# Kernel tuning notes

Measured on AMD Instinct MI355X. Metric: run time of the kernel, lower is better.

The kernel has to match this reference:

```python
import jax, jax.numpy as jnp
import numpy as np

D = 1024          # node_vec_size = 16 heads * 64 head_size
HEADS = 16
DH = 64
HID = 4096        # TFM_HIDDEN_SIZE
L = 12            # TFM_NUM_LAYERS
NC = 256          # num concepts present (WMG2_MAX_CONCEPTS)
CSZ = 128         # WMG2_CONCEPT_SIZE
MAX_AGE = 256     # WMG2_MAX_AGE
AGE_V = MAX_AGE + 2  # 258
OBS = 2048
OUT = 512         # WMG2_OUTPUT_LAYER_SIZE
SCALE = 0.02


def setup_inputs() -> dict:
    key = jax.random.key(0)
    ks = iter(jax.random.split(key, 40))
    rn = lambda shape: jax.random.normal(next(ks), shape, dtype=jnp.float32) * SCALE
    inp = {
        'observation': jax.random.normal(next(ks), (OBS,), dtype=jnp.float32),
        'concepts': jax.random.normal(next(ks), (NC, CSZ), dtype=jnp.float32),
        'W_core': rn((D, OBS)), 'b_core': jnp.zeros((D,), jnp.float32),
        'W_cemb': rn((D, CSZ)), 'b_cemb': jnp.zeros((D,), jnp.float32),
        'W_age': rn((D, AGE_V)), 'b_age': jnp.zeros((D,), jnp.float32),
        'Wq': rn((L, D, D)), 'bq': jnp.zeros((L, D), jnp.float32),
        'Wk': rn((L, D, D)), 'bk': jnp.zeros((L, D), jnp.float32),
        'Wv': rn((L, D, D)), 'bv': jnp.zeros((L, D), jnp.float32),
        'Wo': rn((L, D, D)), 'bo': jnp.zeros((L, D), jnp.float32),
        'ln1_g': jnp.ones((L, D), jnp.float32), 'ln1_b': jnp.zeros((L, D), jnp.float32),
        'W1': rn((L, HID, D)), 'b1': jnp.zeros((L, HID), jnp.float32),
        'W2': rn((L, D, HID)), 'b2': jnp.zeros((L, D), jnp.float32),
        'ln2_g': jnp.ones((L, D), jnp.float32), 'ln2_b': jnp.zeros((L, D), jnp.float32),
        'W_concept': rn((CSZ, D)), 'b_concept': jnp.zeros((CSZ,), jnp.float32),
        'W_out': rn((OUT, D)), 'b_out': jnp.zeros((OUT,), jnp.float32),
    }
    return inp


def _layernorm(x, g, b, eps=1e-5):
    m = jnp.mean(x, axis=-1, keepdims=True)
    v = jnp.var(x, axis=-1, keepdims=True)
    return (x - m) * jax.lax.rsqrt(v + eps) * g + b


def _forward(observation, concepts, W_core, b_core, W_cemb, b_cemb, W_age, b_age,
             Wq, bq, Wk, bk, Wv, bv, Wo, bo, ln1_g, ln1_b, W1, b1, W2, b2,
             ln2_g, ln2_b, W_concept, b_concept, W_out, b_out):
    # --- embed observation node ---
    x0 = observation @ W_core.T + b_core                      # [D]
    # --- embed concept nodes, vectorized age embedding ---
    ages = jnp.arange(NC)
    oh = jax.nn.one_hot(jnp.minimum(ages, AGE_V - 1), AGE_V, dtype=jnp.float32)
    oh = oh.at[:, -1].set(ages.astype(jnp.float32) / MAX_AGE)  # age[-1] = age/MAX_AGE
    age_emb = oh @ W_age.T + b_age                             # [NC, D]
    xc = concepts @ W_cemb.T + b_cemb + age_emb                # [NC, D]
    x = jnp.concatenate([x0[None, :], xc], axis=0)             # [S, D], S = 1+NC

    # --- transformer (post-LN encoder), scan over layers ---
    def layer(h, p):
        wq, bq_, wk, bk_, wv, bv_, wo, bo_, g1, be1, w1, b1_, w2, b2_, g2, be2 = p
        S = h.shape[0]
        q = (h @ wq.T + bq_).reshape(S, HEADS, DH)
        k = (h @ wk.T + bk_).reshape(S, HEADS, DH)
        v = (h @ wv.T + bv_).reshape(S, HEADS, DH)
        scores = jnp.einsum('qhd,khd->hqk', q, k) / jnp.sqrt(jnp.float32(DH))
        attn = jax.nn.softmax(scores, axis=-1)
        o = jnp.einsum('hqk,khd->qhd', attn, v).reshape(S, D)
        h = _layernorm(h + (o @ wo.T + bo_), g1, be1)
        f = jax.nn.relu(h @ w1.T + b1_) @ w2.T + b2_
        h = _layernorm(h + f, g2, be2)
        return h, None

    x, _ = jax.lax.scan(layer, x, (Wq, bq, Wk, bk, Wv, bv, Wo, bo,
                                   ln1_g, ln1_b, W1, b1, W2, b2, ln2_g, ln2_b))
    tfm_out = x[0]                                             # [D] (node 0)
    new_concept = jnp.tanh(tfm_out @ W_concept.T + b_concept)  # [CSZ]
    output = jax.nn.relu(tfm_out @ W_out.T + b_out)[None, :]   # [1, OUT]
    return output, new_concept


def reference(observation, concepts, W_core, b_core, W_cemb, b_cemb, W_age, b_age,
              Wq, bq, Wk, bk, Wv, bv, Wo, bo, ln1_g, ln1_b, W1, b1, W2, b2,
              ln2_g, ln2_b, W_concept, b_concept, W_out, b_out):
    return _forward(observation, concepts, W_core, b_core, W_cemb, b_cemb, W_age, b_age,
                    Wq, bq, Wk, bk, Wv, bv, Wo, bo, ln1_g, ln1_b, W1, b1, W2, b2,
                    ln2_g, ln2_b, W_concept, b_concept, W_out, b_out)
```

## Files before the change

### kernel.cpp

```cpp
#include <hip/hip_runtime.h>
#include <hip/hip_bf16.h>
#include <cmath>

constexpr int D     = 1024;
constexpr int HEADS = 16;
constexpr int DH    = 64;
constexpr int HID   = 4096;
constexpr int NL    = 12;
constexpr int NC    = 256;
constexpr int CSZ   = 128;
constexpr int AGE_V = 258;
constexpr int OBS   = 2048;
constexpr int OUTN  = 512;
constexpr int S     = 257;
constexpr int SP    = 288;

typedef __attribute__((ext_vector_type(8))) short bf16x8v;
typedef __attribute__((ext_vector_type(4))) short short4v;
typedef __attribute__((ext_vector_type(4))) float f32x4;

__device__ __forceinline__ short bfc(float x) {
    __hip_bfloat16 h = __float2bfloat16(x);
    return __builtin_bit_cast(short, h);
}
__device__ __forceinline__ void st_bf16x4(short* p, float4 v) {
    short4v s;
    s.x = bfc(v.x); s.y = bfc(v.y); s.z = bfc(v.z); s.w = bfc(v.w);
    *(short4v*)p = s;
}

constexpr int BM = 96, BN = 32, BK = 64, LDT = 72;

template<int EPI>
__device__ __forceinline__ void gemm_core(const short* __restrict__ A,
                                          const float* __restrict__ B,
                                          const float* __restrict__ bias,
                                          void* __restrict__ Cp,
                                          int K, int N, int kbeg, int klen) {
    __shared__ __align__(16) short As[BM * LDT];
    __shared__ __align__(16) short Bs[BN * LDT];
    const int t  = threadIdx.x;
    const int m0 = blockIdx.y * BM;
    const int n0 = blockIdx.x * BN;
    const int ar = t >> 3;
    const int ac = (t & 7) * 8;
    const short* Ab = A + (size_t)(m0 + ar) * K + kbeg + ac;
    const int sr = t >> 4;
    const int sc = (t & 15) * 4;
    const float* Bb = B + (size_t)(n0 + sr) * K + kbeg + sc;

    const int lane = t & 63, wave = t >> 6;
    const int wm = wave >> 1, wn = wave & 1;
    const int fr = lane & 15, quad = lane >> 4;
    const short* Abase = &As[(wm * 48 + fr) * LDT + quad * 8];
    const short* Bbase = &Bs[(wn * 16 + fr) * LDT + quad * 8];

    f32x4 acc[3] = {};

    bf16x8v areg[3];
    float4  breg[2];
    #pragma unroll
    for (int p = 0; p < 3; ++p)
        areg[p] = *(const bf16x8v*)(Ab + (size_t)(p * 32) * K);
    #pragma unroll
    for (int p = 0; p < 2; ++p)
        breg[p] = *(const float4*)(Bb + (size_t)(p * 16) * K);

    for (int k0 = 0; k0 < klen; k0 += BK) {
        __syncthreads();
        #pragma unroll
        for (int p = 0; p < 3; ++p)
            *(bf16x8v*)&As[(p * 32 + ar) * LDT + ac] = areg[p];
        #pragma unroll
        for (int p = 0; p < 2; ++p)
            st_bf16x4(&Bs[(p * 16 + sr) * LDT + sc], breg[p]);
        __syncthreads();
        if (k0 + BK < klen) {
            #pragma unroll
            for (int p = 0; p < 3; ++p)
                areg[p] = *(const bf16x8v*)(Ab + (size_t)(p * 32) * K + (k0 + BK));
            #pragma unroll
            for (int p = 0; p < 2; ++p)
                breg[p] = *(const float4*)(Bb + (size_t)(p * 16) * K + (k0 + BK));
        }
        #pragma unroll
        for (int kt = 0; kt < 2; ++kt) {
            bf16x8v af[3], bf;
            #pragma unroll
            for (int mt = 0; mt < 3; ++mt)
                af[mt] = *(const bf16x8v*)(Abase + mt * 16 * LDT + kt * 32);
            bf = *(const bf16x8v*)(Bbase + kt * 32);
            #pragma unroll
            for (int mt = 0; mt < 3; ++mt)
                acc[mt] = __builtin_amdgcn_mfma_f32_16x16x32_bf16(
                    af[mt], bf, acc[mt], 0, 0, 0);
        }
    }

    #pragma unroll
    for (int mt = 0; mt < 3; ++mt) {
        const int m = m0 + wm * 48 + mt * 16 + quad * 4;
        const int n = n0 + wn * 16 + fr;
        if (EPI == 2) {
            float* C = (float*)Cp;
            #pragma unroll
            for (int r = 0; r < 4; ++r)
                atomicAdd(&C[(size_t)(m + r) * N + n], acc[mt][r]);
        } else if (EPI == 1) {
            short* C = (short*)Cp;
            const float bvv = bias[n];
            #pragma unroll
            for (int r = 0; r < 4; ++r)
                C[(size_t)(m + r) * N + n] = bfc(fmaxf(acc[mt][r] + bvv, 0.f));
        } else {
            float* C = (float*)Cp;
            const float bvv = bias[n];
            #pragma unroll
            for (int r = 0; r < 4; ++r)
                C[(size_t)(m + r) * N + n] = acc[mt][r] + bvv;
        }
    }
}

template<int EPI>
__global__ __launch_bounds__(256, 3)
void gemm_splitk(const short* __restrict__ A, const float* __restrict__ B,
                 const float* __restrict__ bias, void* __restrict__ C,
                 int K, int N, int klen) {
    gemm_core<EPI>(A, B, bias, C, K, N, blockIdx.z * klen, klen);
}

struct QKVArgs {
    const float* B[3];
    const float* bias[3];
    float* C[3];
};

__global__ __launch_bounds__(256, 3)
void gemm_qkv(const short* __restrict__ A, QKVArgs args, int K, int N) {
    const int z = blockIdx.z;
    gemm_core<0>(A, args.B[z], args.bias[z], args.C[z], K, N, 0, K);
}

constexpr int QB = 8, KT = 32, NT = 9;

__global__ __launch_bounds__(512)
void attn_kernel(const float* __restrict__ Q, const float* __restrict__ Km,
                 const float* __restrict__ V, short* __restrict__ O) {
    __shared__ float Ks[KT * 66];
    __shared__ float Vs[KT * 64];
    __shared__ float pw[QB][NT * KT];
    const int h = blockIdx.y;
    const int t = threadIdx.x;
    const int wq = t >> 6, lane = t & 63;
    const int q = blockIdx.x * QB + wq;
    const bool qok = q < S;
    const int k32 = lane & 31, dh2 = lane >> 5;

    float qr[32];
    #pragma unroll
    for (int i = 0; i < 32; ++i)
        qr[i] = qok ? Q[(size_t)q * D + h * DH + dh2 * 32 + i] : 0.f;

    float s[NT];
    for (int tile = 0; tile < NT; ++tile) {
        const int kk0 = tile * KT;
        __syncthreads();
        #pragma unroll
        for (int p = 0; p < 2; ++p) {
            const int idx = t + p * 512;
            const int kr = idx >> 5, c2 = (idx & 31) * 2;
            const int kg = kk0 + kr;
            float2 v = make_float2(0.f, 0.f);
            if (kg < S) v = *(const float2*)&Km[(size_t)kg * D + h * DH + c2];
            *(float2*)&Ks[kr * 66 + c2] = v;
        }
        __syncthreads();
        float dot = 0.f;
        const float* kp = &Ks[k32 * 66 + dh2 * 32];
        #pragma unroll
        for (int i = 0; i < 32; ++i) dot = fmaf(qr[i], kp[i], dot);
        dot += __shfl_xor(dot, 32, 64);
        s[tile] = (kk0 + k32 < S) ? dot * 0.125f : -1e30f;
    }
    float mx = -1e30f;
    #pragma unroll
    for (int j = 0; j < NT; ++j) mx = fmaxf(mx, s[j]);
    #pragma unroll
    for (int off = 32; off; off >>= 1) mx = fmaxf(mx, __shfl_xor(mx, off, 64));
    float sum = 0.f;
    #pragma unroll
    for (int j = 0; j < NT; ++j) {
        const float e = __expf(s[j] - mx);
        s[j] = e;
        sum += e;
    }
    #pragma unroll
    for (int off = 32; off; off >>= 1) sum += __shfl_xor(sum, off, 64);
    sum *= 0.5f;
    const float inv = 1.f / sum;
    if (qok && dh2 == 0) {
        #pragma unroll
        for (int j = 0; j < NT; ++j) pw[wq][j * KT + k32] = s[j] * inv;
    }
    float acc = 0.f;
    for (int tile = 0; tile < NT; ++tile) {
        const int kk0 = tile * KT;
        __syncthreads();
        {
            const int kr = t >> 4, c4 = (t & 15) * 4;
            const int kg = kk0 + kr;
            float4 v = make_float4(0.f, 0.f, 0.f, 0.f);
            if (kg < S) v = *(const float4*)&V[(size_t)kg * D + h * DH + c4];
            *(float4*)&Vs[kr * 64 + c4] = v;
        }
        __syncthreads();
        if (qok) {
            const float* pwp = &pw[wq][kk0];
            #pragma unroll
            for (int k = 0; k < KT; ++k)
                acc = fmaf(pwp[k], Vs[k * 64 + lane], acc);
        }
    }
    if (qok) O[(size_t)q * D + h * DH + lane] = bfc(acc);
}

__global__ __launch_bounds__(256)
void embed_obs_kernel(const float* __restrict__ obs, const float* __restrict__ Wc,
                      const float* __restrict__ bc, const float* __restrict__ bo0,
                      float* __restrict__ H, short* __restrict__ HB,
                      float* __restrict__ T) {
    const int d = blockIdx.x;
    const int t = threadIdx.x;
    const float4* w4 = (const float4*)&Wc[(size_t)d * OBS];
    const float4* o4 = (const float4*)obs;
    float acc = 0.f;
    #pragma unroll
    for (int i = t; i < OBS / 4; i += 256) {
        const float4 a = o4[i];
        const float4 b = w4[i];
        acc = fmaf(a.x, b.x, acc); acc = fmaf(a.y, b.y, acc);
        acc = fmaf(a.z, b.z, acc); acc = fmaf(a.w, b.w, acc);
    }
    __shared__ float red[256];
    red[t] = acc;
    __syncthreads();
    for (int off = 128; off; off >>= 1) {
        if (t < off) red[t] += red[t + off];
        __syncthreads();
    }
    if (t == 0) {
        const float v = red[0] + bc[d];
        H[d] = v;
        HB[d] = bfc(v);
        T[d] = v + bo0[d];
    }
}

__global__ __launch_bounds__(256)
void embed_concepts_kernel(const float* __restrict__ concepts, const float* __restrict__ Wce,
                           const float* __restrict__ bce, const float* __restrict__ Wa,
                           const float* __restrict__ ba, const float* __restrict__ bo0,
                           float* __restrict__ H, short* __restrict__ HB,
                           short* __restrict__ ATT, float* __restrict__ T) {
    const int row = blockIdx.x + 1;
    const int d = blockIdx.y * 256 + threadIdx.x;
    if (row > NC) {
        H[(size_t)row * D + d] = 0.f;
        HB[(size_t)row * D + d] = 0;
        ATT[(size_t)row * D + d] = 0;
        T[(size_t)row * D + d] = bo0[d];
        return;
    }
    const int i = row - 1;
    __shared__ __align__(16) float cs[CSZ];
    if (threadIdx.x < CSZ) cs[threadIdx.x] = concepts[(size_t)i * CSZ + threadIdx.x];
    __syncthreads();
    const float4* w4 = (const float4*)&Wce[(size_t)d * CSZ];
    const float4* c4 = (const float4*)cs;
    float acc = 0.f;
    #pragma unroll
    for (int c = 0; c < CSZ / 4; ++c) {
        const float4 a = c4[c];
        const float4 b = w4[c];
        acc = fmaf(a.x, b.x, acc); acc = fmaf(a.y, b.y, acc);
        acc = fmaf(a.z, b.z, acc); acc = fmaf(a.w, b.w, acc);
    }
    const float age = Wa[(size_t)d * AGE_V + i] +
                      ((float)i / 256.f) * Wa[(size_t)d * AGE_V + (AGE_V - 1)];
    const float v = acc + bce[d] + ba[d] + age;
    H[(size_t)row * D + d] = v;
    HB[(size_t)row * D + d] = bfc(v);
    T[(size_t)row * D + d] = v + bo0[d];
}

__global__ __launch_bounds__(256)
void ln_kernel(const float* __restrict__ X, const float* __restrict__ g,
               const float* __restrict__ b, float* __restrict__ Y,
               short* __restrict__ Yb,
               float* __restrict__ Tinit, const float* __restrict__ nbias) {
    const int r = blockIdx.x;
    const int t = threadIdx.x;
    const float* x = X + (size_t)r * D;
    float sm = 0.f, ss = 0.f;
    float v[4];
    #pragma unroll
    for (int j = 0; j < 4; ++j) {
        const float u = x[t + j * 256];
        v[j] = u;
        sm += u;
        ss = fmaf(u, u, ss);
    }
    __shared__ float r1[256], r2[256];
    r1[t] = sm; r2[t] = ss;
    __syncthreads();
    for (int off = 128; off; off >>= 1) {
        if (t < off) { r1[t] += r1[t + off]; r2[t] += r2[t + off]; }
        __syncthreads();
    }
    const float m   = r1[0] * (1.f / D);
    const float var = r2[0] * (1.f / D) - m * m;
    const float rs  = rsqrtf(var + 1e-5f);
    #pragma unroll
    for (int j = 0; j < 4; ++j) {
        const int idx = t + j * 256;
        const float y = (v[j] - m) * rs * g[idx] + b[idx];
        Y[(size_t)r * D + idx] = y;
        Yb[(size_t)r * D + idx] = bfc(y);
        if (Tinit) Tinit[(size_t)r * D + idx] = y + nbias[idx];
    }
}

__global__ __launch_bounds__(256)
void head_kernel(const float* __restrict__ H, const float* __restrict__ Wout,
                 const float* __restrict__ bout, const float* __restrict__ Wcon,
                 const float* __restrict__ bcon, float* __restrict__ out) {
    const int j = blockIdx.x;
    const int t = threadIdx.x;
    const float* w = (j < OUTN) ? &Wout[(size_t)j * D] : &Wcon[(size_t)(j - OUTN) * D];
    const float4* w4 = (const float4*)w;
    const float4* h4 = (const float4*)H;
    const float4 a = h4[t];
    const float4 b = w4[t];
    float acc = a.x * b.x + a.y * b.y + a.z * b.z + a.w * b.w;
    __shared__ float red[256];
    red[t] = acc;
    __syncthreads();
    for (int off = 128; off; off >>= 1) {
        if (t < off) red[t] += red[t + off];
        __syncthreads();
    }
    if (t == 0) {
        const float v = red[0] + ((j < OUTN) ? bout[j] : bcon[j - OUTN]);
        out[j] = (j < OUTN) ? fmaxf(v, 0.f) : tanhf(v);
    }
}

extern "C" void kernel_launch(void* const* d_in, const int* in_sizes, int n_in,
                              void* d_out, int out_size, void* d_ws, size_t ws_size,
                              hipStream_t stream) {
    (void)in_sizes; (void)n_in; (void)out_size; (void)ws_size;
    const float* obs     = (const float*)d_in[0];
    const float* concepts= (const float*)d_in[1];
    const float* W_core  = (const float*)d_in[2];
    const float* b_core  = (const float*)d_in[3];
    const float* W_cemb  = (const float*)d_in[4];
    const float* b_cemb  = (const float*)d_in[5];
    const float* W_age   = (const float*)d_in[6];
    const float* b_age   = (const float*)d_in[7];
    const float* Wq      = (const float*)d_in[8];
    const float* bq      = (const float*)d_in[9];
    const float* Wk      = (const float*)d_in[10];
    const float* bk      = (const float*)d_in[11];
    const float* Wv      = (const float*)d_in[12];
    const float* bv      = (const float*)d_in[13];
    const float* Wo      = (const float*)d_in[14];
    const float* bo      = (const float*)d_in[15];
    const float* ln1g    = (const float*)d_in[16];
    const float* ln1b    = (const float*)d_in[17];
    const float* W1      = (const float*)d_in[18];
    const float* b1      = (const float*)d_in[19];
    const float* W2      = (const float*)d_in[20];
    const float* b2      = (const float*)d_in[21];
    const float* ln2g    = (const float*)d_in[22];
    const float* ln2b    = (const float*)d_in[23];
    const float* W_con   = (const float*)d_in[24];
    const float* b_con   = (const float*)d_in[25];
    const float* W_out   = (const float*)d_in[26];
    const float* b_out   = (const float*)d_in[27];
    float* outp = (float*)d_out;

    float* ws   = (float*)d_ws;
    float* h    = ws;
    float* tmpA = h    + (size_t)SP * D;
    float* tmpB = tmpA + (size_t)SP * D;
    float* qb   = tmpB + (size_t)SP * D;
    float* kb   = qb   + (size_t)SP * D;
    float* vb   = kb   + (size_t)SP * D;
    short* hb   = (short*)(vb + (size_t)SP * D);
    short* att  = hb  + (size_t)SP * D;
    short* mid  = att + (size_t)SP * D;

    embed_obs_kernel<<<dim3(D), 256, 0, stream>>>(obs, W_core, b_core, bo, h, hb, tmpA);
    embed_concepts_kernel<<<dim3(SP - 1, D / 256), 256, 0, stream>>>(
        concepts, W_cemb, b_cemb, W_age, b_age, bo, h, hb, att, tmpA);

    for (int l = 0; l < NL; ++l) {
        QKVArgs qa;
        qa.B[0] = Wq + (size_t)l * D * D;  qa.bias[0] = bq + (size_t)l * D;  qa.C[0] = qb;
        qa.B[1] = Wk + (size_t)l * D * D;  qa.bias[1] = bk + (size_t)l * D;  qa.C[1] = kb;
        qa.B[2] = Wv + (size_t)l * D * D;  qa.bias[2] = bv + (size_t)l * D;  qa.C[2] = vb;
        gemm_qkv<<<dim3(D / BN, SP / BM, 3), 256, 0, stream>>>(hb, qa, D, D);
        attn_kernel<<<dim3((S + QB - 1) / QB, HEADS), 512, 0, stream>>>(qb, kb, vb, att);
        gemm_splitk<2><<<dim3(D / BN, SP / BM, 4), 256, 0, stream>>>(
            att, Wo + (size_t)l * D * D, nullptr, tmpA, D, D, 256);
        ln_kernel<<<dim3(S), 256, 0, stream>>>(tmpA, ln1g + (size_t)l * D,
                                               ln1b + (size_t)l * D, h, hb,
                                               tmpB, b2 + (size_t)l * D);
        gemm_splitk<1><<<dim3(HID / BN, SP / BM, 1), 256, 0, stream>>>(
            hb, W1 + (size_t)l * HID * D, b1 + (size_t)l * HID, mid, D, HID, D);
        gemm_splitk<2><<<dim3(D / BN, SP / BM, 8), 256, 0, stream>>>(
            mid, W2 + (size_t)l * D * HID, nullptr, tmpB, HID, D, 512);
        float* ti = (l + 1 < NL) ? tmpA : nullptr;
        const float* nb = (l + 1 < NL) ? (bo + (size_t)(l + 1) * D) : nullptr;
        ln_kernel<<<dim3(S), 256, 0, stream>>>(tmpB, ln2g + (size_t)l * D,
                                               ln2b + (size_t)l * D, h, hb, ti, nb);
    }
    head_kernel<<<dim3(OUTN + CSZ), 256, 0, stream>>>(h, W_out, b_out, W_con, b_con, outp);
}
```

Baseline: 1.541 ms.

## Fuse LayerNorm into following GEMM A-loads and merge embed kernels

Removes the standalone layernorm kernels by computing per-row mean and rstd inside the QKV and W1 GEMMs. Those GEMMs then normalize the fp32 residual tile on the fly while converting it to bf16 for the MFMA tiles, and a few blocks also write the residual-plus-next-bias buffer. The two embedding kernels are merged into one launch, the head kernel absorbs the final layernorm, and BK grows from 64 to 128. This cuts launches and intermediate traffic. In exchange, every GEMM block recomputes row statistics redundantly, reads fp32 A instead of bf16, and runs at lower occupancy (launch bounds of 2 instead of 3).

Result: slower. 1.957 ms (+27.0%).

```diff
diff --git a/kernel.cpp b/kernel.cpp
--- a/kernel.cpp
+++ b/kernel.cpp
@@ -29,71 +29,164 @@
     *(short4v*)p = s;
 }
 
-constexpr int BM = 96, BN = 32, BK = 64, LDT = 72;
-
-template<int EPI>
+constexpr int BM = 96, BN = 32, BK = 128, LDT = 136;
+
+template<int EPI, bool LNA>
 __device__ __forceinline__ void gemm_core(const short* __restrict__ A,
-                                          const float* __restrict__ B,
+                                          const float* __restrict__ Xf,
+                                          const float* __restrict__ lng,
+                                          const float* __restrict__ lnb,
+                                          const float* __restrict__ resb,
+                                          float* __restrict__ resd,
+                                          int resid_sub,
+                                          const float* __restrict__ Bm,
                                           const float* __restrict__ bias,
                                           void* __restrict__ Cp,
-                                          int K, int N, int kbeg, int klen) {
+                                          int K, int N, int kbeg, int klen,
+                                          int m0, int n0, int t) {
     __shared__ __align__(16) short As[BM * LDT];
     __shared__ __align__(16) short Bs[BN * LDT];
-    const int t  = threadIdx.x;
-    const int m0 = blockIdx.y * BM;
-    const int n0 = blockIdx.x * BN;
-    const int ar = t >> 3;
-    const int ac = (t & 7) * 8;
-    const short* Ab = A + (size_t)(m0 + ar) * K + kbeg + ac;
-    const int sr = t >> 4;
-    const int sc = (t & 15) * 4;
-    const float* Bb = B + (size_t)(n0 + sr) * K + kbeg + sc;
-
+    __shared__ float s_mu[BM], s_ri[BM];
     const int lane = t & 63, wave = t >> 6;
+    const int ar  = t >> 4;
+    const int ac8 = (t & 15) * 8;
+    const short* Ab = LNA ? nullptr : (A + (size_t)(m0 + ar) * K + kbeg + ac8);
+    const float* Xa = LNA ? (Xf + (size_t)(m0 + ar) * K + kbeg + ac8) : nullptr;
+    const int sr = t >> 5;
+    const int sc = (t & 31) * 4;
+    const float* Bb = Bm + (size_t)(n0 + sr) * K + kbeg + sc;
+
     const int wm = wave >> 1, wn = wave & 1;
     const int fr = lane & 15, quad = lane >> 4;
     const short* Abase = &As[(wm * 48 + fr) * LDT + quad * 8];
     const short* Bbase = &Bs[(wn * 16 + fr) * LDT + quad * 8];
 
     f32x4 acc[3] = {};
-
-    bf16x8v areg[3];
-    float4  breg[2];
-    #pragma unroll
-    for (int p = 0; p < 3; ++p)
-        areg[p] = *(const bf16x8v*)(Ab + (size_t)(p * 32) * K);
-    #pragma unroll
-    for (int p = 0; p < 2; ++p)
-        breg[p] = *(const float4*)(Bb + (size_t)(p * 16) * K);
+    bf16x8v araw[6];
+    float4  aln[12];
+    float4  breg[4];
+
+    if constexpr (LNA) {
+        #pragma unroll
+        for (int p = 0; p < 6; ++p) {
+            const float* src = Xa + (size_t)(p * 16) * K;
+            aln[2 * p]     = *(const float4*)(src);
+            aln[2 * p + 1] = *(const float4*)(src + 4);
+        }
+    } else {
+        #pragma unroll
+        for (int p = 0; p < 6; ++p)
+            araw[p] = *(const bf16x8v*)(Ab + (size_t)(p * 16) * K);
+    }
+    #pragma unroll
+    for (int p = 0; p < 4; ++p)
+        breg[p] = *(const float4*)(Bb + (size_t)(p * 8) * K);
+
+    if constexpr (LNA) {
+        #pragma unroll 2
+        for (int i = 0; i < 24; ++i) {
+            const int r = wave * 24 + i;
+            const float4* xr = (const float4*)(Xf + (size_t)(m0 + r) * K);
+            float sm = 0.f, ss = 0.f;
+            #pragma unroll
+            for (int j = 0; j < 4; ++j) {
+                const float4 x = xr[lane * 4 + j];
+                sm += x.x + x.y + x.z + x.w;
+                ss = fmaf(x.x, x.x, fmaf(x.y, x.y, fmaf(x.z, x.z, fmaf(x.w, x.w, ss))));
+            }
+            #pragma unroll
+            for (int off = 32; off; off >>= 1) {
+                sm += __shfl_xor(sm, off, 64);
+                ss += __shfl_xor(ss, off, 64);
+            }
+            if (lane == 0) {
+                const float mu = sm * (1.f / 1024.f);
+                s_mu[r] = mu;
+                s_ri[r] = rsqrtf(ss * (1.f / 1024.f) - mu * mu + 1e-5f);
+            }
+        }
+        __syncthreads();
+        if (resid_sub >= 0) {
+            const int rbase = resid_sub * 24;
+            #pragma unroll 4
+            for (int i = 0; i < 24; ++i) {
+                const int rl = rbase + i;
+                const int c = t * 4;
+                const float4 x  = *(const float4*)(Xf + (size_t)(m0 + rl) * K + c);
+                const float4 g4 = *(const float4*)(lng + c);
+                const float4 b4 = *(const float4*)(lnb + c);
+                const float4 n4 = *(const float4*)(resb + c);
+                const float mu = s_mu[rl], ri = s_ri[rl];
+                float4 y;
+                y.x = fmaf((x.x - mu) * ri, g4.x, b4.x) + n4.x;
+                y.y = fmaf((x.y - mu) * ri, g4.y, b4.y) + n4.y;
+                y.z = fmaf((x.z - mu) * ri, g4.z, b4.z) + n4.z;
+                y.w = fmaf((x.w - mu) * ri, g4.w, b4.w) + n4.w;
+                *(float4*)(resd + (size_t)(m0 + rl) * D + c) = y;
+            }
+        }
+    }
 
     for (int k0 = 0; k0 < klen; k0 += BK) {
         __syncthreads();
-        #pragma unroll
-        for (int p = 0; p < 3; ++p)
-            *(bf16x8v*)&As[(p * 32 + ar) * LDT + ac] = areg[p];
-        #pragma unroll
-        for (int p = 0; p < 2; ++p)
-            st_bf16x4(&Bs[(p * 16 + sr) * LDT + sc], breg[p]);
+        if constexpr (LNA) {
+            const float4 g0 = *(const float4*)(lng + kbeg + k0 + ac8);
+            const float4 g1 = *(const float4*)(lng + kbeg + k0 + ac8 + 4);
+            const float4 b0 = *(const float4*)(lnb + kbeg + k0 + ac8);
+            const float4 b1 = *(const float4*)(lnb + kbeg + k0 + ac8 + 4);
+            #pragma unroll
+            for (int p = 0; p < 6; ++p) {
+                const int r = p * 16 + ar;
+                const float mu = s_mu[r], ri = s_ri[r];
+                const float4 xa = aln[2 * p], xb = aln[2 * p + 1];
+                bf16x8v o;
+                o[0] = bfc(fmaf((xa.x - mu) * ri, g0.x, b0.x));
+                o[1] = bfc(fmaf((xa.y - mu) * ri, g0.y, b0.y));
+                o[2] = bfc(fmaf((xa.z - mu) * ri, g0.z, b0.z));
+                o[3] = bfc(fmaf((xa.w - mu) * ri, g0.w, b0.w));
+                o[4] = bfc(fmaf((xb.x - mu) * ri, g1.x, b1.x));
+                o[5] = bfc(fmaf((xb.y - mu) * ri, g1.y, b1.y));
+                o[6] = bfc(fmaf((xb.z - mu) * ri, g1.z, b1.z));
+                o[7] = bfc(fmaf((xb.w - mu) * ri, g1.w, b1.w));
+                *(bf16x8v*)&As[r * LDT + ac8] = o;
+            }
+        } else {
+            #pragma unroll
+            for (int p = 0; p < 6; ++p)
+                *(bf16x8v*)&As[(p * 16 + ar) * LDT + ac8] = araw[p];
+        }
+        #pragma unroll
+        for (int p = 0; p < 4; ++p)
+            st_bf16x4(&Bs[(p * 8 + sr) * LDT + sc], breg[p]);
         __syncthreads();
         if (k0 + BK < klen) {
-            #pragma unroll
-            for (int p = 0; p < 3; ++p)
-                areg[p] = *(const bf16x8v*)(Ab + (size_t)(p * 32) * K + (k0 + BK));
-            #pragma unroll
-            for (int p = 0; p < 2; ++p)
-                breg[p] = *(const float4*)(Bb + (size_t)(p * 16) * K + (k0 + BK));
-        }
-        #pragma unroll
-        for (int kt = 0; kt < 2; ++kt) {
-            bf16x8v af[3], bf;
+            if constexpr (LNA) {
+                #pragma unroll
+                for (int p = 0; p < 6; ++p) {
+                    const float* src = Xa + (size_t)(p * 16) * K + (k0 + BK);
+                    aln[2 * p]     = *(const float4*)(src);
+                    aln[2 * p + 1] = *(const float4*)(src + 4);
+                }
+            } else {
+                #pragma unroll
+                for (int p = 0; p < 6; ++p)
+                    araw[p] = *(const bf16x8v*)(Ab + (size_t)(p * 16) * K + (k0 + BK));
+            }
+            #pragma unroll
+            for (int p = 0; p < 4; ++p)
+                breg[p] = *(const float4*)(Bb + (size_t)(p * 8) * K + (k0 + BK));
+        }
+        #pragma unroll
+        for (int kt = 0; kt < 4; ++kt) {
+            bf16x8v af[3], bfv;
             #pragma unroll
             for (int mt = 0; mt < 3; ++mt)
                 af[mt] = *(const bf16x8v*)(Abase + mt * 16 * LDT + kt * 32);
-            bf = *(const bf16x8v*)(Bbase + kt * 32);
+            bfv = *(const bf16x8v*)(Bbase + kt * 32);
             #pragma unroll
             for (int mt = 0; mt < 3; ++mt)
                 acc[mt] = __builtin_amdgcn_mfma_f32_16x16x32_bf16(
-                    af[mt], bf, acc[mt], 0, 0, 0);
+                    af[mt], bfv, acc[mt], 0, 0, 0);
         }
     }
 
@@ -122,31 +215,57 @@
     }
 }
 
-template<int EPI>
-__global__ __launch_bounds__(256, 3)
-void gemm_splitk(const short* __restrict__ A, const float* __restrict__ B,
-                 const float* __restrict__ bias, void* __restrict__ C,
-                 int K, int N, int klen) {
-    gemm_core<EPI>(A, B, bias, C, K, N, blockIdx.z * klen, klen);
-}
-
 struct QKVArgs {
     const float* B[3];
     const float* bias[3];
     float* C[3];
 };
 
+template<int EPI>
 __global__ __launch_bounds__(256, 3)
-void gemm_qkv(const short* __restrict__ A, QKVArgs args, int K, int N) {
+void k_gemm(const short* __restrict__ A, const float* __restrict__ Bm,
+            const float* __restrict__ bias, void* __restrict__ C,
+            int K, int N, int klen) {
+    gemm_core<EPI, false>(A, nullptr, nullptr, nullptr, nullptr, nullptr, -1,
+                          Bm, bias, C, K, N, blockIdx.z * klen, klen,
+                          blockIdx.y * BM, blockIdx.x * BN, threadIdx.x);
+}
+
+__global__ __launch_bounds__(256, 3)
+void k_gemm_qkv(const short* __restrict__ A, QKVArgs args) {
     const int z = blockIdx.z;
-    gemm_core<0>(A, args.B[z], args.bias[z], args.C[z], K, N, 0, K);
+    gemm_core<0, false>(A, nullptr, nullptr, nullptr, nullptr, nullptr, -1,
+                        args.B[z], args.bias[z], args.C[z], D, D, 0, D,
+                        blockIdx.y * BM, blockIdx.x * BN, threadIdx.x);
+}
+
+__global__ __launch_bounds__(256, 2)
+void k_gemm_qkv_ln(const float* __restrict__ X, const float* __restrict__ lng,
+                   const float* __restrict__ lnb, const float* __restrict__ resb,
+                   float* __restrict__ resd, QKVArgs args) {
+    const int z = blockIdx.z;
+    const int rsub = (z == 0 && blockIdx.x < 4) ? (int)blockIdx.x : -1;
+    gemm_core<0, true>(nullptr, X, lng, lnb, resb, resd, rsub,
+                       args.B[z], args.bias[z], args.C[z], D, D, 0, D,
+                       blockIdx.y * BM, blockIdx.x * BN, threadIdx.x);
+}
+
+__global__ __launch_bounds__(256, 2)
+void k_gemm_w1_ln(const float* __restrict__ X, const float* __restrict__ lng,
+                  const float* __restrict__ lnb, const float* __restrict__ resb,
+                  float* __restrict__ resd, const float* __restrict__ Bm,
+                  const float* __restrict__ bias, short* __restrict__ C) {
+    const int rsub = (blockIdx.x < 4) ? (int)blockIdx.x : -1;
+    gemm_core<1, true>(nullptr, X, lng, lnb, resb, resd, rsub,
+                       Bm, bias, C, D, HID, 0, D,
+                       blockIdx.y * BM, blockIdx.x * BN, threadIdx.x);
 }
 
 constexpr int QB = 8, KT = 32, NT = 9;
 
 __global__ __launch_bounds__(512)
-void attn_kernel(const float* __restrict__ Q, const float* __restrict__ Km,
-                 const float* __restrict__ V, short* __restrict__ O) {
+void k_attn(const float* __restrict__ Q, const float* __restrict__ Km,
+            const float* __restrict__ V, short* __restrict__ O) {
     __shared__ float Ks[KT * 66];
     __shared__ float Vs[KT * 64];
     __shared__ float pw[QB][NT * KT];
@@ -226,58 +345,54 @@
 }
 
 __global__ __launch_bounds__(256)
-void embed_obs_kernel(const float* __restrict__ obs, const float* __restrict__ Wc,
-                      const float* __restrict__ bc, const float* __restrict__ bo0,
-                      float* __restrict__ H, short* __restrict__ HB,
-                      float* __restrict__ T) {
-    const int d = blockIdx.x;
+void k_embed(const float* __restrict__ obs, const float* __restrict__ Wc,
+             const float* __restrict__ bc,
+             const float* __restrict__ concepts, const float* __restrict__ Wce,
+             const float* __restrict__ bce, const float* __restrict__ Wa,
+             const float* __restrict__ ba, const float* __restrict__ bo0,
+             short* __restrict__ HB, short* __restrict__ ATT,
+             float* __restrict__ T) {
     const int t = threadIdx.x;
-    const float4* w4 = (const float4*)&Wc[(size_t)d * OBS];
-    const float4* o4 = (const float4*)obs;
-    float acc = 0.f;
-    #pragma unroll
-    for (int i = t; i < OBS / 4; i += 256) {
-        const float4 a = o4[i];
-        const float4 b = w4[i];
-        acc = fmaf(a.x, b.x, acc); acc = fmaf(a.y, b.y, acc);
-        acc = fmaf(a.z, b.z, acc); acc = fmaf(a.w, b.w, acc);
-    }
     __shared__ float red[256];
-    red[t] = acc;
-    __syncthreads();
-    for (int off = 128; off; off >>= 1) {
-        if (t < off) red[t] += red[t + off];
-        __syncthreads();
-    }
-    if (t == 0) {
-        const float v = red[0] + bc[d];
-        H[d] = v;
-        HB[d] = bfc(v);
-        T[d] = v + bo0[d];
-    }
-}
-
-__global__ __launch_bounds__(256)
-void embed_concepts_kernel(const float* __restrict__ concepts, const float* __restrict__ Wce,
-                           const float* __restrict__ bce, const float* __restrict__ Wa,
-                           const float* __restrict__ ba, const float* __restrict__ bo0,
-                           float* __restrict__ H, short* __restrict__ HB,
-                           short* __restrict__ ATT, float* __restrict__ T) {
-    const int row = blockIdx.x + 1;
-    const int d = blockIdx.y * 256 + threadIdx.x;
+    if (blockIdx.x < D) {
+        const int d = blockIdx.x;
+        const float4* w4 = (const float4*)&Wc[(size_t)d * OBS];
+        const float4* o4 = (const float4*)obs;
+        float acc = 0.f;
+        #pragma unroll
+        for (int i = t; i < OBS / 4; i += 256) {
+            const float4 a = o4[i];
+            const float4 b = w4[i];
+            acc = fmaf(a.x, b.x, acc); acc = fmaf(a.y, b.y, acc);
+            acc = fmaf(a.z, b.z, acc); acc = fmaf(a.w, b.w, acc);
+        }
+        red[t] = acc;
+        __syncthreads();
+        for (int off = 128; off; off >>= 1) {
+            if (t < off) red[t] += red[t + off];
+            __syncthreads();
+        }
+        if (t == 0) {
+            const float v = red[0] + bc[d];
+            HB[d] = bfc(v);
+            T[d] = v + bo0[d];
+        }
+        return;
+    }
+    const int j = blockIdx.x - D;
+    const int row = (j % 287) + 1;
+    const int d = (j / 287) * 256 + t;
     if (row > NC) {
-        H[(size_t)row * D + d] = 0.f;
         HB[(size_t)row * D + d] = 0;
         ATT[(size_t)row * D + d] = 0;
         T[(size_t)row * D + d] = bo0[d];
         return;
     }
     const int i = row - 1;
-    __shared__ __align__(16) float cs[CSZ];
-    if (threadIdx.x < CSZ) cs[threadIdx.x] = concepts[(size_t)i * CSZ + threadIdx.x];
+    if (t < CSZ) red[t] = concepts[(size_t)i * CSZ + t];
     __syncthreads();
     const float4* w4 = (const float4*)&Wce[(size_t)d * CSZ];
-    const float4* c4 = (const float4*)cs;
+    const float4* c4 = (const float4*)red;
     float acc = 0.f;
     #pragma unroll
     for (int c = 0; c < CSZ / 4; ++c) {
@@ -289,69 +404,49 @@
     const float age = Wa[(size_t)d * AGE_V + i] +
                       ((float)i / 256.f) * Wa[(size_t)d * AGE_V + (AGE_V - 1)];
     const float v = acc + bce[d] + ba[d] + age;
-    H[(size_t)row * D + d] = v;
     HB[(size_t)row * D + d] = bfc(v);
     T[(size_t)row * D + d] = v + bo0[d];
 }
 
 __global__ __launch_bounds__(256)
-void ln_kernel(const float* __restrict__ X, const float* __restrict__ g,
-               const float* __restrict__ b, float* __restrict__ Y,
-               short* __restrict__ Yb,
-               float* __restrict__ Tinit, const float* __restrict__ nbias) {
-    const int r = blockIdx.x;
+void k_head_ln(const float* __restrict__ X, const float* __restrict__ g,
+               const float* __restrict__ b, const float* __restrict__ Wout,
+               const float* __restrict__ bout, const float* __restrict__ Wcon,
+               const float* __restrict__ bcon, float* __restrict__ out) {
+    const int j = blockIdx.x;
     const int t = threadIdx.x;
-    const float* x = X + (size_t)r * D;
-    float sm = 0.f, ss = 0.f;
-    float v[4];
-    #pragma unroll
-    for (int j = 0; j < 4; ++j) {
-        const float u = x[t + j * 256];
-        v[j] = u;
-        sm += u;
-        ss = fmaf(u, u, ss);
-    }
     __shared__ float r1[256], r2[256];
+    const float4 x = ((const float4*)X)[t];
+    float sm = x.x + x.y + x.z + x.w;
+    float ss = fmaf(x.x, x.x, fmaf(x.y, x.y, fmaf(x.z, x.z, x.w * x.w)));
     r1[t] = sm; r2[t] = ss;
     __syncthreads();
     for (int off = 128; off; off >>= 1) {
         if (t < off) { r1[t] += r1[t + off]; r2[t] += r2[t + off]; }
         __syncthreads();
     }
-    const float m   = r1[0] * (1.f / D);
-    const float var = r2[0] * (1.f / D) - m * m;
-    const float rs  = rsqrtf(var + 1e-5f);
-    #pragma unroll
-    for (int j = 0; j < 4; ++j) {
-        const int idx = t + j * 256;
-        const float y = (v[j] - m) * rs * g[idx] + b[idx];
-        Y[(size_t)r * D + idx] = y;
-        Yb[(size_t)r * D + idx] = bfc(y);
-        if (Tinit) Tinit[(size_t)r * D + idx] = y + nbias[idx];
-    }
-}
-
-__global__ __launch_bounds__(256)
-void head_kernel(const float* __restrict__ H, const float* __restrict__ Wout,
-                 const float* __restrict__ bout, const float* __restrict__ Wcon,
-                 const float* __restrict__ bcon, float* __restrict__ out) {
-    const int j = blockIdx.x;
-    const int t = threadIdx.x;
+    const float mu  = r1[0] * (1.f / D);
+    const float var = r2[0] * (1.f / D) - mu * mu;
+    const float ri  = rsqrtf(var + 1e-5f);
+    const float4 g4 = ((const float4*)g)[t];
+    const float4 b4 = ((const float4*)b)[t];
+    float4 y;
+    y.x = (x.x - mu) * ri * g4.x + b4.x;
+    y.y = (x.y - mu) * ri * g4.y + b4.y;
+    y.z = (x.z - mu) * ri * g4.z + b4.z;
+    y.w = (x.w - mu) * ri * g4.w + b4.w;
     const float* w = (j < OUTN) ? &Wout[(size_t)j * D] : &Wcon[(size_t)(j - OUTN) * D];
-    const float4* w4 = (const float4*)w;
-    const float4* h4 = (const float4*)H;
-    const float4 a = h4[t];
-    const float4 b = w4[t];
-    float acc = a.x * b.x + a.y * b.y + a.z * b.z + a.w * b.w;
-    __shared__ float red[256];
-    red[t] = acc;
+    const float4 w4 = ((const float4*)w)[t];
+    float acc = y.x * w4.x + y.y * w4.y + y.z * w4.z + y.w * w4.w;
+    __syncthreads();
+    r1[t] = acc;
     __syncthreads();
     for (int off = 128; off; off >>= 1) {
-        if (t < off) red[t] += red[t + off];
+        if (t < off) r1[t] += r1[t + off];
         __syncthreads();
     }
     if (t == 0) {
-        const float v = red[0] + ((j < OUTN) ? bout[j] : bcon[j - OUTN]);
+        const float v = r1[0] + ((j < OUTN) ? bout[j] : bcon[j - OUTN]);
         out[j] = (j < OUTN) ? fmaxf(v, 0.f) : tanhf(v);
     }
 }
@@ -391,8 +486,7 @@
     float* outp = (float*)d_out;
 
     float* ws   = (float*)d_ws;
-    float* h    = ws;
-    float* tmpA = h    + (size_t)SP * D;
+    float* tmpA = ws;
     float* tmpB = tmpA + (size_t)SP * D;
     float* qb   = tmpB + (size_t)SP * D;
     float* kb   = qb   + (size_t)SP * D;
@@ -401,30 +495,34 @@
     short* att  = hb  + (size_t)SP * D;
     short* mid  = att + (size_t)SP * D;
 
-    embed_obs_kernel<<<dim3(D), 256, 0, stream>>>(obs, W_core, b_core, bo, h, hb, tmpA);
-    embed_concepts_kernel<<<dim3(SP - 1, D / 256), 256, 0, stream>>>(
-        concepts, W_cemb, b_cemb, W_age, b_age, bo, h, hb, att, tmpA);
+    k_embed<<<dim3(D + 287 * 4), 256, 0, stream>>>(
+        obs, W_core, b_core, concepts, W_cemb, b_cemb, W_age, b_age, bo,
+        hb, att, tmpA);
 
     for (int l = 0; l < NL; ++l) {
+        const size_t lo = (size_t)l * D * D;
         QKVArgs qa;
-        qa.B[0] = Wq + (size_t)l * D * D;  qa.bias[0] = bq + (size_t)l * D;  qa.C[0] = qb;
-        qa.B[1] = Wk + (size_t)l * D * D;  qa.bias[1] = bk + (size_t)l * D;  qa.C[1] = kb;
-        qa.B[2] = Wv + (size_t)l * D * D;  qa.bias[2] = bv + (size_t)l * D;  qa.C[2] = vb;
-        gemm_qkv<<<dim3(D / BN, SP / BM, 3), 256, 0, stream>>>(hb, qa, D, D);
-        attn_kernel<<<dim3((S + QB - 1) / QB, HEADS), 512, 0, stream>>>(qb, kb, vb, att);
-        gemm_splitk<2><<<dim3(D / BN, SP / BM, 4), 256, 0, stream>>>(
-            att, Wo + (size_t)l * D * D, nullptr, tmpA, D, D, 256);
-        ln_kernel<<<dim3(S), 256, 0, stream>>>(tmpA, ln1g + (size_t)l * D,
-                                               ln1b + (size_t)l * D, h, hb,
-                                               tmpB, b2 + (size_t)l * D);
-        gemm_splitk<1><<<dim3(HID / BN, SP / BM, 1), 256, 0, stream>>>(
-            hb, W1 + (size_t)l * HID * D, b1 + (size_t)l * HID, mid, D, HID, D);
-        gemm_splitk<2><<<dim3(D / BN, SP / BM, 8), 256, 0, stream>>>(
+        qa.B[0] = Wq + lo;  qa.bias[0] = bq + (size_t)l * D;  qa.C[0] = qb;
+        qa.B[1] = Wk + lo;  qa.bias[1] = bk + (size_t)l * D;  qa.C[1] = kb;
+        qa.B[2] = Wv + lo;  qa.bias[2] = bv + (size_t)l * D;  qa.C[2] = vb;
+        if (l == 0) {
+            k_gemm_qkv<<<dim3(32, 3, 3), 256, 0, stream>>>(hb, qa);
+        } else {
+            k_gemm_qkv_ln<<<dim3(32, 3, 3), 256, 0, stream>>>(
+                tmpB, ln2g + (size_t)(l - 1) * D, ln2b + (size_t)(l - 1) * D,
+                bo + (size_t)l * D, tmpA, qa);
+        }
+        k_attn<<<dim3((S + QB - 1) / QB, HEADS), 512, 0, stream>>>(qb, kb, vb, att);
+        k_gemm<2><<<dim3(32, 3, 4), 256, 0, stream>>>(
+            att, Wo + lo, nullptr, tmpA, D, D, 256);
+        k_gemm_w1_ln<<<dim3(128, 3), 256, 0, stream>>>(
+            tmpA, ln1g + (size_t)l * D, ln1b + (size_t)l * D,
+            b2 + (size_t)l * D, tmpB,
+            W1 + (size_t)l * HID * D, b1 + (size_t)l * HID, mid);
+        k_gemm<2><<<dim3(32, 3, 8), 256, 0, stream>>>(
             mid, W2 + (size_t)l * D * HID, nullptr, tmpB, HID, D, 512);
-        float* ti = (l + 1 < NL) ? tmpA : nullptr;
-        const float* nb = (l + 1 < NL) ? (bo + (size_t)(l + 1) * D) : nullptr;
-        ln_kernel<<<dim3(S), 256, 0, stream>>>(tmpB, ln2g + (size_t)l * D,
-                                               ln2b + (size_t)l * D, h, hb, ti, nb);
-    }
-    head_kernel<<<dim3(OUTN + CSZ), 256, 0, stream>>>(h, W_out, b_out, W_con, b_con, outp);
-}
+    }
+    k_head_ln<<<dim3(OUTN + CSZ), 256, 0, stream>>>(
+        tmpB, ln2g + (size_t)(NL - 1) * D, ln2b + (size_t)(NL - 1) * D,
+        W_out, b_out, W_con, b_con, outp);
+}
```
